# Performance work log

Hardware: AMD Instinct MI355X
Metric: run time of the kernel (lower is better)

## Reference

```python
import jax, jax.numpy as jnp
import numpy as np

N_NODES = 200000
DIM_NODE = 128
DIM_NIG = 128
DIM_HIDDEN = 256
BATCH = 8192


def setup_inputs() -> dict:
    key = jax.random.key(0)
    ks = jax.random.split(key, 16)
    s = 0.05
    inp = {
        "src_node_ids": jnp.arange(BATCH, dtype=jnp.int64),
        "dst_node_ids": jnp.arange(BATCH, dtype=jnp.int64),
        "src_previous_embedding": jax.random.normal(ks[0], (N_NODES, DIM_NODE), jnp.float32),
        "dst_previous_embedding": jax.random.normal(ks[1], (N_NODES, DIM_NODE), jnp.float32),
        "batch_src_neighbor_embedding": jax.random.normal(ks[2], (BATCH, DIM_NIG), jnp.float32),
        "batch_dst_neighbor_embedding": jax.random.normal(ks[3], (BATCH, DIM_NIG), jnp.float32),
        # Linear params stored as [in, out]; forward is x @ W + b (== torch x @ W_t.T + b)
        "W_src_nig": jax.random.normal(ks[4], (DIM_NIG, DIM_HIDDEN), jnp.float32) * s,
        "b_src_nig": jnp.zeros((DIM_HIDDEN,), jnp.float32),
        "W_src_resize": jax.random.normal(ks[5], (DIM_NODE, DIM_HIDDEN), jnp.float32) * s,
        "b_src_resize": jnp.zeros((DIM_HIDDEN,), jnp.float32),
        "W_src_out": jax.random.normal(ks[6], (2 * DIM_HIDDEN, DIM_NODE), jnp.float32) * s,
        "b_src_out": jnp.zeros((DIM_NODE,), jnp.float32),
        "W_dst_nig": jax.random.normal(ks[7], (DIM_NIG, DIM_HIDDEN), jnp.float32) * s,
        "b_dst_nig": jnp.zeros((DIM_HIDDEN,), jnp.float32),
        "W_dst_resize": jax.random.normal(ks[8], (DIM_NODE, DIM_HIDDEN), jnp.float32) * s,
        "b_dst_resize": jnp.zeros((DIM_HIDDEN,), jnp.float32),
        "W_dst_out": jax.random.normal(ks[9], (2 * DIM_HIDDEN, DIM_NODE), jnp.float32) * s,
        "b_dst_out": jnp.zeros((DIM_NODE,), jnp.float32),
    }
    return inp


def _update_side(ids, prev_emb, nig_emb, W_nig, b_nig, W_resize, b_resize, W_out, b_out):
    # gather rows [B, dim_node] -> resize to hidden
    sel = prev_emb[ids] @ W_resize + b_resize            # [B, H]
    shift = nig_emb @ W_nig + b_nig                      # [B, H]
    node_emb = jnp.concatenate([sel, shift], axis=1) @ W_out + b_out  # [B, dim_node]
    # clone().detach() then scatter-write rows
    return prev_emb.at[ids].set(node_emb)


def reference(src_node_ids, dst_node_ids, src_previous_embedding, dst_previous_embedding,
              batch_src_neighbor_embedding, batch_dst_neighbor_embedding,
              W_src_nig, b_src_nig, W_src_resize, b_src_resize, W_src_out, b_src_out,
              W_dst_nig, b_dst_nig, W_dst_resize, b_dst_resize, W_dst_out, b_dst_out):
    updated_src = _update_side(src_node_ids, src_previous_embedding, batch_src_neighbor_embedding,
                               W_src_nig, b_src_nig, W_src_resize, b_src_resize, W_src_out, b_src_out)
    updated_dst = _update_side(dst_node_ids, dst_previous_embedding, batch_dst_neighbor_embedding,
                               W_dst_nig, b_dst_nig, W_dst_resize, b_dst_resize, W_dst_out, b_dst_out)
    return (updated_src, updated_dst)
```

## Files before the change

kernel.cpp:

```cpp
#include <hip/hip_runtime.h>

#define N_NODES 200000
#define DIM 128
#define HID 256
#define BATCH 8192
#define SIDE_FLOATS (N_NODES * DIM)

__global__ __launch_bounds__(128) void precompute_kernel(
    const float* __restrict__ Wr0, const float* __restrict__ Wn0, const float* __restrict__ Wo0,
    const float* __restrict__ br0, const float* __restrict__ bn0, const float* __restrict__ bo0,
    const float* __restrict__ Wr1, const float* __restrict__ Wn1, const float* __restrict__ Wo1,
    const float* __restrict__ br1, const float* __restrict__ bn1, const float* __restrict__ bo1,
    float* __restrict__ Mf, float* __restrict__ bias)
{
    const int s = blockIdx.y;
    const float* Wr = s ? Wr1 : Wr0;
    const float* Wn = s ? Wn1 : Wn0;
    const float* Wo = s ? Wo1 : Wo0;
    const float* br = s ? br1 : br0;
    const float* bn = s ? bn1 : bn0;
    const float* bo = s ? bo1 : bo0;
    const int j = threadIdx.x;
    const int k = blockIdx.x;

    if (k < 2 * DIM) {
        __shared__ float w[HID];
        const float* wrow = (k < DIM) ? (Wr + k * HID) : (Wn + (k - DIM) * HID);
        const float* wo   = (k < DIM) ? Wo : (Wo + HID * DIM);
        w[j]       = wrow[j];
        w[j + DIM] = wrow[j + DIM];
        __syncthreads();
        float acc = 0.f;
        #pragma unroll 8
        for (int h = 0; h < HID; ++h) acc += w[h] * wo[h * DIM + j];
        Mf[((s << 8) + k) * DIM + j] = acc;
    } else {
        float acc = bo[j];
        for (int h = 0; h < HID; ++h) acc += br[h] * Wo[h * DIM + j];
        for (int h = 0; h < HID; ++h) acc += bn[h] * Wo[(HID + h) * DIM + j];
        bias[s * DIM + j] = acc;
    }
}

__global__ __launch_bounds__(256) void copy_kernel(
    const float4* __restrict__ a, const float4* __restrict__ b,
    float4* __restrict__ out, long n4side)
{
    long i = (long)blockIdx.x * blockDim.x + threadIdx.x;
    const long stride = (long)gridDim.x * blockDim.x;
    const long total = 2 * n4side;
    for (; i < total; i += stride) {
        out[i] = (i < n4side) ? a[i] : b[i - n4side];
    }
}

#define RB 32
#define CAT_STRIDE 260

__global__ __launch_bounds__(256) void update_kernel(
    const int* __restrict__ ids0, const float* __restrict__ prev0, const float* __restrict__ nig0,
    const int* __restrict__ ids1, const float* __restrict__ prev1, const float* __restrict__ nig1,
    const float* __restrict__ Mf, const float* __restrict__ bias,
    float* __restrict__ out)
{
    const int s = blockIdx.y;
    const int*   ids  = s ? ids1  : ids0;
    const float* prev = s ? prev1 : prev0;
    const float* nig  = s ? nig1  : nig0;
    const float* M    = Mf + s * (2 * DIM) * DIM;
    const float* bs   = bias + s * DIM;
    float* outs = out + (size_t)s * SIDE_FLOATS;

    __shared__ int   sid[RB];
    __shared__ float cat[RB][CAT_STRIDE];

    const int tid = threadIdx.x;
    const int b0  = blockIdx.x * RB;

    if (tid < RB) sid[tid] = ids[b0 + tid];
    __syncthreads();

    for (int idx = tid; idx < RB * 64; idx += 256) {
        const int r = idx >> 6;
        const int q = idx & 63;
        float4 v;
        if (q < 32) v = ((const float4*)(prev + (size_t)sid[r] * DIM))[q];
        else        v = ((const float4*)(nig  + (size_t)(b0 + r) * DIM))[q - 32];
        *(float4*)&cat[r][q * 4] = v;
    }
    __syncthreads();

    const int jg = tid & 31;
    const int rg = tid >> 5;

    float acc[4][4];
    #pragma unroll
    for (int r = 0; r < 4; ++r)
        #pragma unroll
        for (int c = 0; c < 4; ++c) acc[r][c] = 0.f;

    const float4* M4 = (const float4*)M;
    #pragma unroll 4
    for (int k = 0; k < 2 * DIM; ++k) {
        const float4 m = M4[(k << 5) + jg];
        #pragma unroll
        for (int r = 0; r < 4; ++r) {
            const float a = cat[rg * 4 + r][k];
            acc[r][0] += a * m.x;
            acc[r][1] += a * m.y;
            acc[r][2] += a * m.z;
            acc[r][3] += a * m.w;
        }
    }

    const float4 bj = ((const float4*)bs)[jg];
    #pragma unroll
    for (int r = 0; r < 4; ++r) {
        const int row = sid[rg * 4 + r];
        float4 v;
        v.x = acc[r][0] + bj.x;
        v.y = acc[r][1] + bj.y;
        v.z = acc[r][2] + bj.z;
        v.w = acc[r][3] + bj.w;
        ((float4*)(outs + (size_t)row * DIM))[jg] = v;
    }
}

extern "C" void kernel_launch(void* const* d_in, const int* in_sizes, int n_in,
                              void* d_out, int out_size, void* d_ws, size_t ws_size,
                              hipStream_t stream) {
    const int*   src_ids   = (const int*)d_in[0];
    const int*   dst_ids   = (const int*)d_in[1];
    const float* src_prev  = (const float*)d_in[2];
    const float* dst_prev  = (const float*)d_in[3];
    const float* src_nig   = (const float*)d_in[4];
    const float* dst_nig   = (const float*)d_in[5];
    const float* W_src_nig     = (const float*)d_in[6];
    const float* b_src_nig     = (const float*)d_in[7];
    const float* W_src_resize  = (const float*)d_in[8];
    const float* b_src_resize  = (const float*)d_in[9];
    const float* W_src_out     = (const float*)d_in[10];
    const float* b_src_out     = (const float*)d_in[11];
    const float* W_dst_nig     = (const float*)d_in[12];
    const float* b_dst_nig     = (const float*)d_in[13];
    const float* W_dst_resize  = (const float*)d_in[14];
    const float* b_dst_resize  = (const float*)d_in[15];
    const float* W_dst_out     = (const float*)d_in[16];
    const float* b_dst_out     = (const float*)d_in[17];

    float* out  = (float*)d_out;
    float* Mf   = (float*)d_ws;
    float* bias = Mf + 2 * (2 * DIM) * DIM;

    precompute_kernel<<<dim3(2 * DIM + 1, 2), 128, 0, stream>>>(
        W_src_resize, W_src_nig, W_src_out, b_src_resize, b_src_nig, b_src_out,
        W_dst_resize, W_dst_nig, W_dst_out, b_dst_resize, b_dst_nig, b_dst_out,
        Mf, bias);

    const long n4side = SIDE_FLOATS / 4;
    copy_kernel<<<4096, 256, 0, stream>>>(
        (const float4*)src_prev, (const float4*)dst_prev, (float4*)out, n4side);

    update_kernel<<<dim3(BATCH / RB, 2), 256, 0, stream>>>(
        src_ids, src_prev, src_nig,
        dst_ids, dst_prev, dst_nig,
        Mf, bias, out);
}
```

Baseline: 436.2 us.

## Fuse table copy with row update using per-node overwrite flags

```diff
diff --git a/kernel.cpp b/kernel.cpp
--- a/kernel.cpp
+++ b/kernel.cpp
@@ -5,25 +5,27 @@
 #define HID 256
 #define BATCH 8192
 #define SIDE_FLOATS (N_NODES * DIM)
+#define MAGIC 0x5EED1234u
 
-__global__ __launch_bounds__(128) void precompute_kernel(
+typedef float vf4 __attribute__((ext_vector_type(4)));
+
+__global__ __launch_bounds__(128) void setup_kernel(
     const float* __restrict__ Wr0, const float* __restrict__ Wn0, const float* __restrict__ Wo0,
     const float* __restrict__ br0, const float* __restrict__ bn0, const float* __restrict__ bo0,
     const float* __restrict__ Wr1, const float* __restrict__ Wn1, const float* __restrict__ Wo1,
     const float* __restrict__ br1, const float* __restrict__ bn1, const float* __restrict__ bo1,
-    float* __restrict__ Mf, float* __restrict__ bias)
+    const int* __restrict__ ids0, const int* __restrict__ ids1,
+    float* __restrict__ Mf, float* __restrict__ bias,
+    unsigned* __restrict__ flags0, unsigned* __restrict__ flags1)
 {
     const int s = blockIdx.y;
-    const float* Wr = s ? Wr1 : Wr0;
-    const float* Wn = s ? Wn1 : Wn0;
-    const float* Wo = s ? Wo1 : Wo0;
-    const float* br = s ? br1 : br0;
-    const float* bn = s ? bn1 : bn0;
-    const float* bo = s ? bo1 : bo0;
     const int j = threadIdx.x;
     const int k = blockIdx.x;
 
     if (k < 2 * DIM) {
+        const float* Wr = s ? Wr1 : Wr0;
+        const float* Wn = s ? Wn1 : Wn0;
+        const float* Wo = s ? Wo1 : Wo0;
         __shared__ float w[HID];
         const float* wrow = (k < DIM) ? (Wr + k * HID) : (Wn + (k - DIM) * HID);
         const float* wo   = (k < DIM) ? Wo : (Wo + HID * DIM);
@@ -34,95 +36,121 @@
         #pragma unroll 8
         for (int h = 0; h < HID; ++h) acc += w[h] * wo[h * DIM + j];
         Mf[((s << 8) + k) * DIM + j] = acc;
-    } else {
+    } else if (k == 2 * DIM) {
+        const float* Wo = s ? Wo1 : Wo0;
+        const float* br = s ? br1 : br0;
+        const float* bn = s ? bn1 : bn0;
+        const float* bo = s ? bo1 : bo0;
         float acc = bo[j];
         for (int h = 0; h < HID; ++h) acc += br[h] * Wo[h * DIM + j];
         for (int h = 0; h < HID; ++h) acc += bn[h] * Wo[(HID + h) * DIM + j];
         bias[s * DIM + j] = acc;
-    }
-}
-
-__global__ __launch_bounds__(256) void copy_kernel(
-    const float4* __restrict__ a, const float4* __restrict__ b,
-    float4* __restrict__ out, long n4side)
-{
-    long i = (long)blockIdx.x * blockDim.x + threadIdx.x;
-    const long stride = (long)gridDim.x * blockDim.x;
-    const long total = 2 * n4side;
-    for (; i < total; i += stride) {
-        out[i] = (i < n4side) ? a[i] : b[i - n4side];
+    } else {
+        const int i = (k - (2 * DIM + 1)) * 128 + j;
+        const int* ids   = s ? ids1 : ids0;
+        unsigned*  fl    = s ? flags1 : flags0;
+        fl[ids[i]] = MAGIC;
     }
 }
 
 #define RB 32
 #define CAT_STRIDE 260
 
-__global__ __launch_bounds__(256) void update_kernel(
+#define COPY_BLOCKS_PER_SIDE 4096
+#define ROW_GROUPS 25000
+
+__global__ __launch_bounds__(256) void fused_kernel(
     const int* __restrict__ ids0, const float* __restrict__ prev0, const float* __restrict__ nig0,
     const int* __restrict__ ids1, const float* __restrict__ prev1, const float* __restrict__ nig1,
     const float* __restrict__ Mf, const float* __restrict__ bias,
+    const unsigned* __restrict__ flags0, const unsigned* __restrict__ flags1,
     float* __restrict__ out)
 {
-    const int s = blockIdx.y;
-    const int*   ids  = s ? ids1  : ids0;
-    const float* prev = s ? prev1 : prev0;
-    const float* nig  = s ? nig1  : nig0;
-    const float* M    = Mf + s * (2 * DIM) * DIM;
-    const float* bs   = bias + s * DIM;
-    float* outs = out + (size_t)s * SIDE_FLOATS;
+    const int bx  = blockIdx.x;
+    const int tid = threadIdx.x;
 
-    __shared__ int   sid[RB];
-    __shared__ float cat[RB][CAT_STRIDE];
+    if (bx < 512) {
+        const int s = bx >> 8;
+        const int*   ids  = s ? ids1  : ids0;
+        const float* prev = s ? prev1 : prev0;
+        const float* nig  = s ? nig1  : nig0;
+        const float* M    = Mf + s * (2 * DIM) * DIM;
+        const float* bs   = bias + s * DIM;
+        float* outs = out + (size_t)s * SIDE_FLOATS;
 
-    const int tid = threadIdx.x;
-    const int b0  = blockIdx.x * RB;
+        __shared__ int   sid[RB];
+        __shared__ float cat[RB][CAT_STRIDE];
 
-    if (tid < RB) sid[tid] = ids[b0 + tid];
-    __syncthreads();
+        const int b0 = (bx & 255) * RB;
 
-    for (int idx = tid; idx < RB * 64; idx += 256) {
-        const int r = idx >> 6;
-        const int q = idx & 63;
-        float4 v;
-        if (q < 32) v = ((const float4*)(prev + (size_t)sid[r] * DIM))[q];
-        else        v = ((const float4*)(nig  + (size_t)(b0 + r) * DIM))[q - 32];
-        *(float4*)&cat[r][q * 4] = v;
-    }
-    __syncthreads();
+        if (tid < RB) sid[tid] = ids[b0 + tid];
+        __syncthreads();
 
-    const int jg = tid & 31;
-    const int rg = tid >> 5;
+        for (int idx = tid; idx < RB * 64; idx += 256) {
+            const int r = idx >> 6;
+            const int q = idx & 63;
+            float4 v;
+            if (q < 32) v = ((const float4*)(prev + (size_t)sid[r] * DIM))[q];
+            else        v = ((const float4*)(nig  + (size_t)(b0 + r) * DIM))[q - 32];
+            *(float4*)&cat[r][q * 4] = v;
+        }
+        __syncthreads();
 
-    float acc[4][4];
-    #pragma unroll
-    for (int r = 0; r < 4; ++r)
+        const int jg = tid & 31;
+        const int rg = tid >> 5;
+
+        float acc[4][4];
         #pragma unroll
-        for (int c = 0; c < 4; ++c) acc[r][c] = 0.f;
+        for (int r = 0; r < 4; ++r)
+            #pragma unroll
+            for (int c = 0; c < 4; ++c) acc[r][c] = 0.f;
 
-    const float4* M4 = (const float4*)M;
-    #pragma unroll 4
-    for (int k = 0; k < 2 * DIM; ++k) {
-        const float4 m = M4[(k << 5) + jg];
+        const float4* M4 = (const float4*)M;
+        #pragma unroll 4
+        for (int k = 0; k < 2 * DIM; ++k) {
+            const float4 m = M4[(k << 5) + jg];
+            #pragma unroll
+            for (int r = 0; r < 4; ++r) {
+                const float a = cat[rg * 4 + r][k];
+                acc[r][0] += a * m.x;
+                acc[r][1] += a * m.y;
+                acc[r][2] += a * m.z;
+                acc[r][3] += a * m.w;
+            }
+        }
+
+        const float4 bj = ((const float4*)bs)[jg];
         #pragma unroll
         for (int r = 0; r < 4; ++r) {
-            const float a = cat[rg * 4 + r][k];
-            acc[r][0] += a * m.x;
-            acc[r][1] += a * m.y;
-            acc[r][2] += a * m.z;
-            acc[r][3] += a * m.w;
+            const int row = sid[rg * 4 + r];
+            float4 v;
+            v.x = acc[r][0] + bj.x;
+            v.y = acc[r][1] + bj.y;
+            v.z = acc[r][2] + bj.z;
+            v.w = acc[r][3] + bj.w;
+            ((float4*)(outs + (size_t)row * DIM))[jg] = v;
         }
+        return;
     }
 
-    const float4 bj = ((const float4*)bs)[jg];
-    #pragma unroll
-    for (int r = 0; r < 4; ++r) {
-        const int row = sid[rg * 4 + r];
-        float4 v;
-        v.x = acc[r][0] + bj.x;
-        v.y = acc[r][1] + bj.y;
-        v.z = acc[r][2] + bj.z;
-        v.w = acc[r][3] + bj.w;
-        ((float4*)(outs + (size_t)row * DIM))[jg] = v;
+    const int cb   = bx - 512;
+    const int side = cb >> 12;
+    const int c    = cb & (COPY_BLOCKS_PER_SIDE - 1);
+    const vf4*      p4 = (const vf4*)(side ? prev1 : prev0);
+    const unsigned* fl = side ? flags1 : flags0;
+    vf4* o4 = (vf4*)out + (size_t)side * (SIDE_FLOATS / 4);
+
+    const int rloc = tid >> 5;
+    const int q    = tid & 31;
+
+    #pragma unroll 2
+    for (int g = c; g < ROW_GROUPS; g += COPY_BLOCKS_PER_SIDE) {
+        const int row = (g << 3) + rloc;
+        if (fl[row] != MAGIC) {
+            const size_t idx = (size_t)row * 32 + q;
+            vf4 v = __builtin_nontemporal_load(p4 + idx);
+            __builtin_nontemporal_store(v, o4 + idx);
+        }
     }
 }
 
@@ -151,18 +179,16 @@
     float* out  = (float*)d_out;
     float* Mf   = (float*)d_ws;
     float* bias = Mf + 2 * (2 * DIM) * DIM;
+    unsigned* flags0 = (unsigned*)(bias + 2 * DIM);
+    unsigned* flags1 = flags0 + N_NODES;
 
-    precompute_kernel<<<dim3(2 * DIM + 1, 2), 128, 0, stream>>>(
+    setup_kernel<<<dim3(2 * DIM + 1 + BATCH / 128, 2), 128, 0, stream>>>(
         W_src_resize, W_src_nig, W_src_out, b_src_resize, b_src_nig, b_src_out,
         W_dst_resize, W_dst_nig, W_dst_out, b_dst_resize, b_dst_nig, b_dst_out,
-        Mf, bias);
+        src_ids, dst_ids, Mf, bias, flags0, flags1);
 
-    const long n4side = SIDE_FLOATS / 4;
-    copy_kernel<<<4096, 256, 0, stream>>>(
-        (const float4*)src_prev, (const float4*)dst_prev, (float4*)out, n4side);
-
-    update_kernel<<<dim3(BATCH / RB, 2), 256, 0, stream>>>(
+    fused_kernel<<<512 + 2 * COPY_BLOCKS_PER_SIDE, 256, 0, stream>>>(
         src_ids, src_prev, src_nig,
         dst_ids, dst_prev, dst_nig,
-        Mf, bias, out);
+        Mf, bias, flags0, flags1, out);
 }
```

After: 404.8 us. 1.08x faster.
